# Kernel tuning notes

Measured on AMD Instinct MI355X. Metric: run time of the kernel, lower is better.

The kernel has to match this reference:

```python
import jax, jax.numpy as jnp
import numpy as np

N_NODES = 1_000_000
N_EDGES = 4_000_000
N_GRAPHS = 32768
IN_DIM, HID = 7, 128
BN_EPS = 1e-5


def setup_inputs() -> dict:
    key = jax.random.key(0)
    ks = iter(jax.random.split(key, 32))
    x = jax.random.normal(next(ks), (N_NODES, IN_DIM), jnp.float32)
    edge_index = jax.random.randint(next(ks), (2, N_EDGES), 0, N_NODES, dtype=jnp.int32)
    batch = jnp.sort(jax.random.randint(next(ks), (N_NODES,), 0, N_GRAPHS, dtype=jnp.int32))

    def lin_w(kk, fi, fo):  # torch nn.Linear-style init
        return (jax.random.uniform(kk, (fi, fo), jnp.float32) * 2.0 - 1.0) / np.float32(np.sqrt(fi))

    inp = {"x": x, "edge_index": edge_index, "batch": batch}
    dims = [(IN_DIM, HID), (HID, HID), (HID, HID)]
    for i, (fi, fo) in enumerate(dims, 1):
        inp[f"W{i}"] = lin_w(next(ks), fi, fo)
        inp[f"b{i}"] = jnp.zeros((fo,), jnp.float32)
        inp[f"gamma{i}"] = 1.0 + 0.1 * jax.random.normal(next(ks), (fo,), jnp.float32)
        inp[f"beta{i}"] = 0.1 * jax.random.normal(next(ks), (fo,), jnp.float32)
        inp[f"rmean{i}"] = jnp.zeros((fo,), jnp.float32)
        inp[f"rvar{i}"] = jnp.ones((fo,), jnp.float32)
    inp["Wc1"] = lin_w(next(ks), HID, HID // 2)
    inp["bc1"] = jnp.zeros((HID // 2,), jnp.float32)
    inp["Wc2"] = lin_w(next(ks), HID // 2, 1)
    inp["bc2"] = jnp.zeros((1,), jnp.float32)
    return inp


def _gcn_norm(edge_index, n):
    # PyG GCNConv: add self-loops, symmetric D^{-1/2} A D^{-1/2} normalization.
    loops = jnp.arange(n, dtype=edge_index.dtype)
    src = jnp.concatenate([edge_index[0], loops])
    dst = jnp.concatenate([edge_index[1], loops])
    deg = jax.ops.segment_sum(jnp.ones_like(dst, jnp.float32), dst, num_segments=n)
    dinv = jnp.where(deg > 0, jax.lax.rsqrt(deg), 0.0)
    return src, dst, dinv[src] * dinv[dst]


def reference(x, edge_index, batch,
              W1, b1, gamma1, beta1, rmean1, rvar1,
              W2, b2, gamma2, beta2, rmean2, rvar2,
              W3, b3, gamma3, beta3, rmean3, rvar3,
              Wc1, bc1, Wc2, bc2):
    n = x.shape[0]
    src, dst, norm = _gcn_norm(edge_index, n)
    layers = [(W1, b1, gamma1, beta1, rmean1, rvar1),
              (W2, b2, gamma2, beta2, rmean2, rvar2),
              (W3, b3, gamma3, beta3, rmean3, rvar3)]
    h = x
    for W, b, g, bt, rm, rv in layers:
        h = h @ W                                                   # [N, H]
        h = jax.ops.segment_sum(h[src] * norm[:, None], dst, num_segments=n) + b
        h = (h - rm) * jax.lax.rsqrt(rv + BN_EPS) * g + bt          # BatchNorm1d (eval)
        h = jax.nn.relu(h)                                          # dropout = identity in eval
    cnt = jax.ops.segment_sum(jnp.ones((n,), jnp.float32), batch, num_segments=N_GRAPHS)
    pooled = jax.ops.segment_sum(h, batch, num_segments=N_GRAPHS) / jnp.maximum(cnt, 1.0)[:, None]
    hidden = jax.nn.relu(pooled @ Wc1 + bc1)
    logits = (hidden @ Wc2 + bc2).squeeze(-1)                       # [N_GRAPHS]
    return logits
```

## Files before the change

kernel.cpp:

```cpp
#include <hip/hip_runtime.h>
#include <hip/hip_fp16.h>

#define N_NODES 1000000
#define N_EDGES 4000000
#define N_GRAPHS 32768
#define BN_EPS 1e-5f
#define NBLK1 3907

typedef _Float16 f16;
typedef f16   f16x8 __attribute__((ext_vector_type(8)));
typedef float f32x4 __attribute__((ext_vector_type(4)));
typedef float f32x2 __attribute__((ext_vector_type(2)));

__device__ __half g_hA[128000000];
__device__ __half g_hB[128000000];
__device__ float  g_agg7[8400000];
__device__ float  g_dinv[N_NODES];
__device__ int    g_rowcnt[N_NODES];
__device__ int    g_row_start[N_NODES + 1];
__device__ int    g_csr_src[N_EDGES];
__device__ int    g_part[NBLK1];
__device__ int    g_gstart[N_GRAPHS + 1];
__device__ __align__(16) __half g_wt1[4096];
__device__ __align__(16) __half g_wt2[16384];
__device__ __align__(16) __half g_wt3[16384];


__device__ __forceinline__ void set8(uint4 raw, float f[8]) {
    __half2 h; float2 a;
    __builtin_memcpy(&h, &raw.x, 4); a = __half22float2(h); f[0] = a.x; f[1] = a.y;
    __builtin_memcpy(&h, &raw.y, 4); a = __half22float2(h); f[2] = a.x; f[3] = a.y;
    __builtin_memcpy(&h, &raw.z, 4); a = __half22float2(h); f[4] = a.x; f[5] = a.y;
    __builtin_memcpy(&h, &raw.w, 4); a = __half22float2(h); f[6] = a.x; f[7] = a.y;
}
__device__ __forceinline__ uint4 pack8(const float f[8]) {
    __half2 h0 = __floats2half2_rn(f[0], f[1]);
    __half2 h1 = __floats2half2_rn(f[2], f[3]);
    __half2 h2 = __floats2half2_rn(f[4], f[5]);
    __half2 h3 = __floats2half2_rn(f[6], f[7]);
    uint4 raw;
    __builtin_memcpy(&raw.x, &h0, 4);
    __builtin_memcpy(&raw.y, &h1, 4);
    __builtin_memcpy(&raw.z, &h2, 4);
    __builtin_memcpy(&raw.w, &h3, 4);
    return raw;
}
__device__ __forceinline__ f32x2 cvt2h(unsigned raw) {
    __half2 h; __builtin_memcpy(&h, &raw, 4);
    float2 a = __half22float2(h);
    f32x2 r; r.x = a.x; r.y = a.y; return r;
}


__device__ __forceinline__ void set8_fp8v(uint2 raw, f32x2 f[4]) {
    f[0] = __builtin_amdgcn_cvt_pk_f32_fp8(raw.x, false);
    f[1] = __builtin_amdgcn_cvt_pk_f32_fp8(raw.x, true);
    f[2] = __builtin_amdgcn_cvt_pk_f32_fp8(raw.y, false);
    f[3] = __builtin_amdgcn_cvt_pk_f32_fp8(raw.y, true);
}
__device__ __forceinline__ void add8_fp8v(uint2 raw, f32x2 f[4]) {
    f[0] += __builtin_amdgcn_cvt_pk_f32_fp8(raw.x, false);
    f[1] += __builtin_amdgcn_cvt_pk_f32_fp8(raw.x, true);
    f[2] += __builtin_amdgcn_cvt_pk_f32_fp8(raw.y, false);
    f[3] += __builtin_amdgcn_cvt_pk_f32_fp8(raw.y, true);
}
__device__ __forceinline__ uint4 pack8v(const f32x2 f[4]) {
    __half2 h0 = __floats2half2_rn(f[0].x, f[0].y);
    __half2 h1 = __floats2half2_rn(f[1].x, f[1].y);
    __half2 h2 = __floats2half2_rn(f[2].x, f[2].y);
    __half2 h3 = __floats2half2_rn(f[3].x, f[3].y);
    uint4 raw;
    __builtin_memcpy(&raw.x, &h0, 4);
    __builtin_memcpy(&raw.y, &h1, 4);
    __builtin_memcpy(&raw.z, &h2, 4);
    __builtin_memcpy(&raw.w, &h3, 4);
    return raw;
}
__device__ __forceinline__ uint2 pack8_fp8(const float f[8]) {
    int lo = 0, hi = 0;
    lo = __builtin_amdgcn_cvt_pk_fp8_f32(f[0], f[1], lo, false);
    lo = __builtin_amdgcn_cvt_pk_fp8_f32(f[2], f[3], lo, true);
    hi = __builtin_amdgcn_cvt_pk_fp8_f32(f[4], f[5], hi, false);
    hi = __builtin_amdgcn_cvt_pk_fp8_f32(f[6], f[7], hi, true);
    uint2 r; r.x = (unsigned)lo; r.y = (unsigned)hi; return r;
}


__global__ __launch_bounds__(256) void k_prep(const float* __restrict__ W1,
                                              const float* __restrict__ W2,
                                              const float* __restrict__ W3) {
    int t = blockIdx.x * 256 + threadIdx.x;
    if (t < N_NODES) { g_rowcnt[t] = 0; return; }
    int u = t - N_NODES;
    if (u < 32768) {
        int sel = u >> 14, v = u & 16383;
        int n = v & 127, k = v >> 7;
        (sel ? g_wt3 : g_wt2)[n * 128 + k] = __float2half_rn((sel ? W3 : W2)[k * 128 + n]);
        return;
    }
    u -= 32768;
    if (u < 4096) {
        int n = u & 127, k = u >> 7;
        g_wt1[n * 32 + k] = (k < 7) ? __float2half_rn(W1[k * 128 + n]) : __float2half_rn(0.f);
    }
}


__global__ __launch_bounds__(256) void k_hist(const int* __restrict__ dst) {
    int e = blockIdx.x * 256 + threadIdx.x;
    if (e < N_EDGES) atomicAdd(&g_rowcnt[dst[e]], 1);
}

__global__ __launch_bounds__(256) void k_scan1(const float* __restrict__ x) {
    __shared__ int sh[256];
    int i = blockIdx.x * 256 + threadIdx.x;
    int v = (i < N_NODES) ? g_rowcnt[i] : 0;
    if (i < N_NODES) {
        float w = rsqrtf((float)(1 + v));
        g_dinv[i] = w;
        float vv[8];
#pragma unroll
        for (int k = 0; k < 7; ++k) vv[k] = x[i * 7 + k] * w;
        vv[7] = 0.f;
        *(uint4*)(g_hB + (size_t)i * 8) = pack8(vv);
    }
    sh[threadIdx.x] = v;
    __syncthreads();
#pragma unroll
    for (int off = 1; off < 256; off <<= 1) {
        int t = (threadIdx.x >= off) ? sh[threadIdx.x - off] : 0;
        __syncthreads();
        sh[threadIdx.x] += t;
        __syncthreads();
    }
    int incl = sh[threadIdx.x];
    if (i < N_NODES) g_row_start[i] = incl - v;
    if (threadIdx.x == 255) g_part[blockIdx.x] = incl;
}

__global__ __launch_bounds__(256) void k_scan2() {
    __shared__ int sh[256];
    int base = threadIdx.x * 16;
    int local[16];
    int s = 0;
#pragma unroll
    for (int k = 0; k < 16; ++k) {
        local[k] = (base + k < NBLK1) ? g_part[base + k] : 0;
        s += local[k];
    }
    sh[threadIdx.x] = s;
    __syncthreads();
#pragma unroll
    for (int off = 1; off < 256; off <<= 1) {
        int t = (threadIdx.x >= off) ? sh[threadIdx.x - off] : 0;
        __syncthreads();
        sh[threadIdx.x] += t;
        __syncthreads();
    }
    int carry = sh[threadIdx.x] - s;
#pragma unroll
    for (int k = 0; k < 16; ++k) {
        if (base + k < NBLK1) {
            int t = local[k];
            g_part[base + k] = carry;
            carry += t;
        }
    }
}

__global__ __launch_bounds__(256) void k_scan3() {
    int i = blockIdx.x * 256 + threadIdx.x;
    if (i < N_NODES) {
        g_row_start[i] += g_part[blockIdx.x];
        g_rowcnt[i] = 0;
    }
    if (i == 0) g_row_start[N_NODES] = N_EDGES;
}

__global__ __launch_bounds__(256) void k_scatter(const int* __restrict__ src,
                                                 const int* __restrict__ dst) {
    int e = blockIdx.x * 256 + threadIdx.x;
    if (e >= N_EDGES) return;
    int d = dst[e];
    int pos = g_row_start[d] + atomicAdd(&g_rowcnt[d], 1);
    g_csr_src[pos] = src[e];
}


__global__ __launch_bounds__(256) void k_gz(const int* __restrict__ batch) {
    int blk = blockIdx.x;
    if (blk < 4096) {
        int t = blk * 256 + threadIdx.x;
        *(float4*)(g_agg7 + (size_t)t * 4) = make_float4(0.f, 0.f, 0.f, 0.f);
        return;
    }
    int gidx = (blk - 4096) * 256 + threadIdx.x;
    if (gidx > N_GRAPHS) return;
    int lo = 0, hi = N_NODES;
    while (lo < hi) {
        int mid = (lo + hi) >> 1;
        if (batch[mid] < gidx) lo = mid + 1; else hi = mid;
    }
    g_gstart[gidx] = lo;
}


__global__ __launch_bounds__(256, 7) void k_l1_fused(const float* __restrict__ b,
                                                     const float* __restrict__ g,
                                                     const float* __restrict__ bt,
                                                     const float* __restrict__ rm,
                                                     const float* __restrict__ rv) {
    const __half* __restrict__ px = g_hB;
    unsigned char* __restrict__ q1 = (unsigned char*)g_hA;

    __shared__ __half As[64][152];
    const int tid = threadIdx.x;
    const int node0 = blockIdx.x * 64;

    {
        const int slot = tid >> 2;
        const int q = tid & 3;
        int i = node0 + slot;
        f32x2 f = cvt2h(*(const unsigned*)(px + (size_t)i * 8 + q * 2));
        int e = g_row_start[i], e1 = g_row_start[i + 1];
        for (; e + 4 <= e1; e += 4) {
            int s0 = g_csr_src[e + 0], s1 = g_csr_src[e + 1];
            int s2 = g_csr_src[e + 2], s3 = g_csr_src[e + 3];
            unsigned r0 = *(const unsigned*)(px + (size_t)s0 * 8 + q * 2);
            unsigned r1 = *(const unsigned*)(px + (size_t)s1 * 8 + q * 2);
            unsigned r2 = *(const unsigned*)(px + (size_t)s2 * 8 + q * 2);
            unsigned r3 = *(const unsigned*)(px + (size_t)s3 * 8 + q * 2);
            f += cvt2h(r0); f += cvt2h(r1); f += cvt2h(r2); f += cvt2h(r3);
        }
        for (; e < e1; ++e)
            f += cvt2h(*(const unsigned*)(px + (size_t)g_csr_src[e] * 8 + q * 2));
        __half2 hv = __floats2half2_rn(f.x, f.y);
        unsigned u; __builtin_memcpy(&u, &hv, 4);
        *(unsigned*)(&As[slot][q * 2]) = u;
        uint4 z; z.x = 0; z.y = 0; z.z = 0; z.w = 0;
        *(uint4*)(&As[slot][8 + q * 8]) = z;
    }

    const int wv = tid >> 6;
    const int lane = tid & 63;
    const int lm = lane & 15;
    const int lq = lane >> 4;

    __syncthreads();

    f32x4 acc[4][2];
#pragma unroll
    for (int mt = 0; mt < 4; ++mt)
#pragma unroll
        for (int nt = 0; nt < 2; ++nt) acc[mt][nt] = (f32x4){0.f, 0.f, 0.f, 0.f};

    f16x8 bq[2];
#pragma unroll
    for (int nt = 0; nt < 2; ++nt)
        __builtin_memcpy(&bq[nt], g_wt1 + (size_t)(wv * 32 + nt * 16 + lm) * 32 + lq * 8, 16);
#pragma unroll
    for (int mt = 0; mt < 4; ++mt) {
        f16x8 afr;
        __builtin_memcpy(&afr, &As[mt * 16 + lm][lq * 8], 16);
#pragma unroll
        for (int nt = 0; nt < 2; ++nt)
            acc[mt][nt] = __builtin_amdgcn_mfma_f32_16x16x32_f16(afr, bq[nt], acc[mt][nt], 0, 0, 0);
    }

    float4 dv4[4];
#pragma unroll
    for (int mt = 0; mt < 4; ++mt)
        dv4[mt] = *(const float4*)(g_dinv + node0 + mt * 16 + lq * 4);

    __syncthreads();

#pragma unroll
    for (int nt = 0; nt < 2; ++nt) {
        int c = wv * 32 + nt * 16 + lm;
        float s = g[c] * rsqrtf(rv[c] + BN_EPS);
        float o = fmaf(b[c] - rm[c], s, bt[c]);
#pragma unroll
        for (int mt = 0; mt < 4; ++mt) {
            float dvr[4] = {dv4[mt].x, dv4[mt].y, dv4[mt].z, dv4[mt].w};
#pragma unroll
            for (int r = 0; r < 4; ++r) {
                float y = fmaxf(fmaf(acc[mt][nt][r] * dvr[r], s, o), 0.f) * dvr[r];
                As[mt * 16 + lq * 4 + r][c] = __float2half_rn(y);
            }
        }
    }
    __syncthreads();
#pragma unroll
    for (int i = 0; i < 2; ++i) {
        int u = tid + i * 256;
        int row = u >> 3, cb = (u & 7) * 16;
        float fa[8], fb[8];
        set8(*(const uint4*)(&As[row][cb]), fa);
        set8(*(const uint4*)(&As[row][cb + 8]), fb);
        uint2 pa = pack8_fp8(fa), pb = pack8_fp8(fb);
        uint4 v; v.x = pa.x; v.y = pa.y; v.z = pb.x; v.w = pb.y;
        *(uint4*)(q1 + (size_t)(node0 + row) * 128 + cb) = v;
    }
}


template <bool PRE, bool ATOB, int WSEL, int OUTMODE>
__global__ __launch_bounds__(256, 7) void k_agg_gemm(const float* __restrict__ b,
                                                     const float* __restrict__ g,
                                                     const float* __restrict__ bt,
                                                     const float* __restrict__ rm,
                                                     const float* __restrict__ rv,
                                                     const int* __restrict__ batch) {
    const unsigned char* __restrict__ hin8 =
        (const unsigned char*)(ATOB ? g_hA : g_hB);
    unsigned char* __restrict__ hout8 =
        (unsigned char*)(ATOB ? g_hB : g_hA);
    const __half* __restrict__ WtG = (WSEL == 0) ? g_wt2 : g_wt3;

    __shared__ __half As[64][152];
    __shared__ int bsh[64];
    const int tid = threadIdx.x;
    const int node0 = blockIdx.x * 64;

    {
        const int slot = tid >> 4;
        const int c0 = (tid & 15) * 8;
#pragma unroll
        for (int pair = 0; pair < 2; ++pair) {
            const int iA = node0 + (pair * 2 + 0) * 16 + slot;
            const int iB = node0 + (pair * 2 + 1) * 16 + slot;
            f32x2 fA[4], fB[4];
            set8_fp8v(*(const uint2*)(hin8 + (size_t)iA * 128 + c0), fA);
            set8_fp8v(*(const uint2*)(hin8 + (size_t)iB * 128 + c0), fB);
            const int eA = g_row_start[iA], e1A = g_row_start[iA + 1];
            const int eB = g_row_start[iB], e1B = g_row_start[iB + 1];
            const int emA = min(max(e1A - 1, eA), N_EDGES - 1);
            const int emB = min(max(e1B - 1, eB), N_EDGES - 1);
            const int dmax = max(e1A - eA, e1B - eB);
            for (int done = 0; done < dmax; done += 4) {
                const int bA = eA + done, bB = eB + done;
                int sA0 = g_csr_src[min(bA,     emA)];
                int sA1 = g_csr_src[min(bA + 1, emA)];
                int sA2 = g_csr_src[min(bA + 2, emA)];
                int sA3 = g_csr_src[min(bA + 3, emA)];
                int sB0 = g_csr_src[min(bB,     emB)];
                int sB1 = g_csr_src[min(bB + 1, emB)];
                int sB2 = g_csr_src[min(bB + 2, emB)];
                int sB3 = g_csr_src[min(bB + 3, emB)];
                uint2 rA0 = *(const uint2*)(hin8 + (size_t)sA0 * 128 + c0);
                uint2 rA1 = *(const uint2*)(hin8 + (size_t)sA1 * 128 + c0);
                uint2 rA2 = *(const uint2*)(hin8 + (size_t)sA2 * 128 + c0);
                uint2 rA3 = *(const uint2*)(hin8 + (size_t)sA3 * 128 + c0);
                uint2 rB0 = *(const uint2*)(hin8 + (size_t)sB0 * 128 + c0);
                uint2 rB1 = *(const uint2*)(hin8 + (size_t)sB1 * 128 + c0);
                uint2 rB2 = *(const uint2*)(hin8 + (size_t)sB2 * 128 + c0);
                uint2 rB3 = *(const uint2*)(hin8 + (size_t)sB3 * 128 + c0);
                __builtin_amdgcn_sched_barrier(0);
                if (bA     >= e1A) { rA0.x = 0u; rA0.y = 0u; }
                if (bA + 1 >= e1A) { rA1.x = 0u; rA1.y = 0u; }
                if (bA + 2 >= e1A) { rA2.x = 0u; rA2.y = 0u; }
                if (bA + 3 >= e1A) { rA3.x = 0u; rA3.y = 0u; }
                if (bB     >= e1B) { rB0.x = 0u; rB0.y = 0u; }
                if (bB + 1 >= e1B) { rB1.x = 0u; rB1.y = 0u; }
                if (bB + 2 >= e1B) { rB2.x = 0u; rB2.y = 0u; }
                if (bB + 3 >= e1B) { rB3.x = 0u; rB3.y = 0u; }
                add8_fp8v(rA0, fA); add8_fp8v(rA1, fA); add8_fp8v(rA2, fA); add8_fp8v(rA3, fA);
                add8_fp8v(rB0, fB); add8_fp8v(rB1, fB); add8_fp8v(rB2, fB); add8_fp8v(rB3, fB);
            }
            *(uint4*)(&As[(pair * 2 + 0) * 16 + slot][c0]) = pack8v(fA);
            *(uint4*)(&As[(pair * 2 + 1) * 16 + slot][c0]) = pack8v(fB);
        }
    }

    const int wv = tid >> 6;
    const int lane = tid & 63;
    const int lm = lane & 15;
    const int lq = lane >> 4;

    __syncthreads();

    f32x4 acc[4][2];
#pragma unroll
    for (int mt = 0; mt < 4; ++mt)
#pragma unroll
        for (int nt = 0; nt < 2; ++nt) acc[mt][nt] = (f32x4){0.f, 0.f, 0.f, 0.f};

#pragma unroll
    for (int kb = 0; kb < 4; ++kb) {
        f16x8 bq[2];
#pragma unroll
        for (int nt = 0; nt < 2; ++nt)
            __builtin_memcpy(&bq[nt],
                             WtG + (size_t)(wv * 32 + nt * 16 + lm) * 128 + kb * 32 + lq * 8, 16);
#pragma unroll
        for (int mt = 0; mt < 4; ++mt) {
            f16x8 afr;
            __builtin_memcpy(&afr, &As[mt * 16 + lm][kb * 32 + lq * 8], 16);
#pragma unroll
            for (int nt = 0; nt < 2; ++nt)
                acc[mt][nt] = __builtin_amdgcn_mfma_f32_16x16x32_f16(afr, bq[nt], acc[mt][nt], 0, 0, 0);
        }
    }

    float4 dv4[4];
#pragma unroll
    for (int mt = 0; mt < 4; ++mt)
        dv4[mt] = *(const float4*)(g_dinv + node0 + mt * 16 + lq * 4);

    if (OUTMODE == 2 && tid < 64) bsh[tid] = batch[node0 + tid];

    __syncthreads();

#pragma unroll
    for (int nt = 0; nt < 2; ++nt) {
        int c = wv * 32 + nt * 16 + lm;
        float s = g[c] * rsqrtf(rv[c] + BN_EPS);
        float o = fmaf(b[c] - rm[c], s, bt[c]);
#pragma unroll
        for (int mt = 0; mt < 4; ++mt) {
            float dvr[4] = {dv4[mt].x, dv4[mt].y, dv4[mt].z, dv4[mt].w};
#pragma unroll
            for (int r = 0; r < 4; ++r) {
                float pm = PRE ? dvr[r] : 1.0f;
                float y = fmaxf(fmaf(acc[mt][nt][r] * dvr[r], s, o), 0.f) * pm;
                As[mt * 16 + lq * 4 + r][c] = __float2half_rn(y);
            }
        }
    }
    __syncthreads();

    if (OUTMODE == 1) {
#pragma unroll
        for (int i = 0; i < 2; ++i) {
            int u = tid + i * 256;
            int row = u >> 3, cb = (u & 7) * 16;
            float fa[8], fb[8];
            set8(*(const uint4*)(&As[row][cb]), fa);
            set8(*(const uint4*)(&As[row][cb + 8]), fb);
            uint2 pa = pack8_fp8(fa), pb = pack8_fp8(fb);
            uint4 v; v.x = pa.x; v.y = pa.y; v.z = pb.x; v.w = pb.y;
            *(uint4*)(hout8 + (size_t)(node0 + row) * 128 + cb) = v;
        }
    } else {
        const int c = tid & 127;
        const int r0 = (tid >> 7) * 32;
        float accp = 0.f;
        int g0 = bsh[r0];
        for (int row = r0; row < r0 + 32; ++row) {
            int gg = bsh[row];
            if (gg != g0) {
                atomicAdd(&g_agg7[(size_t)g0 * 128 + c], accp);
                accp = 0.f; g0 = gg;
            }
            accp += __half2float(As[row][c]);
        }
        atomicAdd(&g_agg7[(size_t)g0 * 128 + c], accp);
    }
}


__global__ __launch_bounds__(256) void k_head(const float* __restrict__ Wc1,
                                              const float* __restrict__ bc1,
                                              const float* __restrict__ Wc2,
                                              const float* __restrict__ bc2,
                                              float* __restrict__ out) {
    __shared__ float hsh[4][64];
    const int g4 = blockIdx.x * 4;
    const int gi = g4 + (threadIdx.x >> 6);
    const int c = threadIdx.x & 63;
    const float* pooled = g_agg7;
    int cnt = g_gstart[gi + 1] - g_gstart[gi];
    float inv = 1.0f / (float)max(cnt, 1);
    float z = 0.f;
#pragma unroll 8
    for (int k = 0; k < 128; ++k) z = fmaf(pooled[(size_t)gi * 128 + k], Wc1[k * 64 + c], z);
    hsh[threadIdx.x >> 6][c] = fmaxf(fmaf(z, inv, bc1[c]), 0.f);
    __syncthreads();
    if (threadIdx.x < 4) {
        float zz = bc2[0];
#pragma unroll 8
        for (int k = 0; k < 64; ++k) zz = fmaf(hsh[threadIdx.x][k], Wc2[k], zz);
        out[g4 + threadIdx.x] = zz;
    }
}


extern "C" void kernel_launch(void* const* d_in, const int* in_sizes, int n_in,
                              void* d_out, int out_size, void* d_ws, size_t ws_size,
                              hipStream_t stream) {
    const float* x     = (const float*)d_in[0];
    const int*   ei    = (const int*)d_in[1];
    const int*   batch = (const int*)d_in[2];
    const float* W1 = (const float*)d_in[3];
    const float* b1 = (const float*)d_in[4];
    const float* g1 = (const float*)d_in[5];
    const float* bt1= (const float*)d_in[6];
    const float* rm1= (const float*)d_in[7];
    const float* rv1= (const float*)d_in[8];
    const float* W2 = (const float*)d_in[9];
    const float* b2 = (const float*)d_in[10];
    const float* g2 = (const float*)d_in[11];
    const float* bt2= (const float*)d_in[12];
    const float* rm2= (const float*)d_in[13];
    const float* rv2= (const float*)d_in[14];
    const float* W3 = (const float*)d_in[15];
    const float* b3 = (const float*)d_in[16];
    const float* g3 = (const float*)d_in[17];
    const float* bt3= (const float*)d_in[18];
    const float* rm3= (const float*)d_in[19];
    const float* rv3= (const float*)d_in[20];
    const float* Wc1= (const float*)d_in[21];
    const float* bc1= (const float*)d_in[22];
    const float* Wc2= (const float*)d_in[23];
    const float* bc2= (const float*)d_in[24];
    float* outp = (float*)d_out;
    (void)d_ws; (void)ws_size; (void)n_in; (void)in_sizes;

    const int* srcp = ei;
    const int* dstp = ei + N_EDGES;

    k_prep<<<4051, 256, 0, stream>>>(W1, W2, W3);

    k_hist<<<(N_EDGES + 255) / 256, 256, 0, stream>>>(dstp);
    k_scan1<<<NBLK1, 256, 0, stream>>>(x);
    k_scan2<<<1, 256, 0, stream>>>();
    k_scan3<<<NBLK1, 256, 0, stream>>>();
    k_scatter<<<(N_EDGES + 255) / 256, 256, 0, stream>>>(srcp, dstp);

    k_gz<<<4225, 256, 0, stream>>>(batch);

    k_l1_fused<<<N_NODES / 64, 256, 0, stream>>>(b1, g1, bt1, rm1, rv1);

    k_agg_gemm<true,  true,  0, 1><<<N_NODES / 64, 256, 0, stream>>>(b2, g2, bt2, rm2, rv2, batch);
    k_agg_gemm<false, false, 1, 2><<<N_NODES / 64, 256, 0, stream>>>(b3, g3, bt3, rm3, rv3, batch);

    k_head<<<N_GRAPHS / 4, 256, 0, stream>>>(Wc1, bc1, Wc2, bc2, outp);
}
```

Measured before the change: 1.062 ms.

## Build CSR via two-level bucket sort with shared-memory atomics

Replaces the global-atomic histogram and scatter used for CSR construction with a two-pass bucketed approach. Edges are first binned into 256 coarse destination buckets, using block-local lists and then global appends. Per-bucket blocks then count degrees and place sources using shared-memory atomics. The aim is to cut scattered global atomics and random writes, at the cost of an extra packed-pair buffer and more kernel launches. Only 256 blocks run the per-bucket kernels, which limits parallelism on a large GPU.

```diff
diff --git a/kernel.cpp b/kernel.cpp
--- a/kernel.cpp
+++ b/kernel.cpp
@@ -6,6 +6,11 @@
 #define N_GRAPHS 32768
 #define BN_EPS 1e-5f
 #define NBLK1 3907
+#define NB 256
+#define BKT_SHIFT 12
+#define EPB 2048
+#define NSCAT 1954
+#define CAPB 32
 
 typedef _Float16 f16;
 typedef f16   f16x8 __attribute__((ext_vector_type(8)));
@@ -19,8 +24,12 @@
 __device__ int    g_rowcnt[N_NODES];
 __device__ int    g_row_start[N_NODES + 1];
 __device__ int    g_csr_src[N_EDGES];
+__device__ unsigned g_pairs[N_EDGES];
 __device__ int    g_part[NBLK1];
 __device__ int    g_gstart[N_GRAPHS + 1];
+__device__ int    g_bcnt[NB];
+__device__ int    g_bstart[NB + 1];
+__device__ int    g_bcur[NB];
 __device__ __align__(16) __half g_wt1[4096];
 __device__ __align__(16) __half g_wt2[16384];
 __device__ __align__(16) __half g_wt3[16384];
@@ -102,13 +111,104 @@
     if (u < 4096) {
         int n = u & 127, k = u >> 7;
         g_wt1[n * 32 + k] = (k < 7) ? __float2half_rn(W1[k * 128 + n]) : __float2half_rn(0.f);
-    }
-}
-
-
-__global__ __launch_bounds__(256) void k_hist(const int* __restrict__ dst) {
-    int e = blockIdx.x * 256 + threadIdx.x;
-    if (e < N_EDGES) atomicAdd(&g_rowcnt[dst[e]], 1);
+        return;
+    }
+    u -= 4096;
+    if (u < NB) g_bcnt[u] = 0;
+}
+
+
+__global__ __launch_bounds__(256) void k_bhist(const int* __restrict__ dst) {
+    __shared__ int h[NB];
+    h[threadIdx.x] = 0;
+    __syncthreads();
+    int base = blockIdx.x * EPB;
+#pragma unroll
+    for (int k = 0; k < 8; ++k) {
+        int e = base + k * 256 + threadIdx.x;
+        if (e < N_EDGES) atomicAdd(&h[((unsigned)dst[e]) >> BKT_SHIFT], 1);
+    }
+    __syncthreads();
+    int c = h[threadIdx.x];
+    if (c) atomicAdd(&g_bcnt[threadIdx.x], c);
+}
+
+__global__ __launch_bounds__(256) void k_bscan() {
+    __shared__ int sh[256];
+    int v = g_bcnt[threadIdx.x];
+    sh[threadIdx.x] = v;
+    __syncthreads();
+#pragma unroll
+    for (int off = 1; off < 256; off <<= 1) {
+        int t = (threadIdx.x >= off) ? sh[threadIdx.x - off] : 0;
+        __syncthreads();
+        sh[threadIdx.x] += t;
+        __syncthreads();
+    }
+    int excl = sh[threadIdx.x] - v;
+    g_bstart[threadIdx.x] = excl;
+    g_bcur[threadIdx.x] = excl;
+    if (threadIdx.x == 255) g_bstart[NB] = N_EDGES;
+}
+
+__global__ __launch_bounds__(256) void k_bscatter(const int* __restrict__ src,
+                                                  const int* __restrict__ dst) {
+    __shared__ int lcnt[NB];
+    __shared__ unsigned llist[NB][CAPB];
+    lcnt[threadIdx.x] = 0;
+    __syncthreads();
+    int base = blockIdx.x * EPB;
+#pragma unroll
+    for (int k = 0; k < 8; ++k) {
+        int e = base + k * 256 + threadIdx.x;
+        if (e < N_EDGES) {
+            unsigned d = (unsigned)dst[e];
+            unsigned p = (((unsigned)src[e]) << BKT_SHIFT) | (d & 4095u);
+            int b = (int)(d >> BKT_SHIFT);
+            int slot = atomicAdd(&lcnt[b], 1);
+            if (slot < CAPB) llist[b][slot] = p;
+            else {
+                int gpos = atomicAdd(&g_bcur[b], 1);
+                g_pairs[gpos] = p;
+            }
+        }
+    }
+    __syncthreads();
+    int c = min(lcnt[threadIdx.x], CAPB);
+    if (c > 0) {
+        int gbase = atomicAdd(&g_bcur[threadIdx.x], c);
+        for (int i = 0; i < c; ++i) g_pairs[gbase + i] = llist[threadIdx.x][i];
+    }
+}
+
+__global__ __launch_bounds__(256) void k_bdeg() {
+    __shared__ int cnt[4096];
+    const int b = blockIdx.x;
+    for (int j = threadIdx.x; j < 4096; j += 256) cnt[j] = 0;
+    __syncthreads();
+    const int s0 = g_bstart[b], s1 = g_bstart[b + 1];
+    for (int i = s0 + threadIdx.x; i < s1; i += 256)
+        atomicAdd(&cnt[g_pairs[i] & 4095u], 1);
+    __syncthreads();
+    const int n0 = b << BKT_SHIFT;
+    for (int j = threadIdx.x; j < 4096; j += 256)
+        if (n0 + j < N_NODES) g_rowcnt[n0 + j] = cnt[j];
+}
+
+__global__ __launch_bounds__(256) void k_bcsr() {
+    __shared__ int cnt[4096];
+    const int b = blockIdx.x;
+    for (int j = threadIdx.x; j < 4096; j += 256) cnt[j] = 0;
+    __syncthreads();
+    const int s0 = g_bstart[b], s1 = g_bstart[b + 1];
+    const int n0 = b << BKT_SHIFT;
+    for (int i = s0 + threadIdx.x; i < s1; i += 256) {
+        unsigned p = g_pairs[i];
+        int dl = (int)(p & 4095u);
+        int off = atomicAdd(&cnt[dl], 1);
+        int pos = g_row_start[n0 + dl] + off;
+        g_csr_src[pos] = (int)(p >> BKT_SHIFT);
+    }
 }
 
 __global__ __launch_bounds__(256) void k_scan1(const float* __restrict__ x) {
@@ -170,20 +270,8 @@
 
 __global__ __launch_bounds__(256) void k_scan3() {
     int i = blockIdx.x * 256 + threadIdx.x;
-    if (i < N_NODES) {
-        g_row_start[i] += g_part[blockIdx.x];
-        g_rowcnt[i] = 0;
-    }
+    if (i < N_NODES) g_row_start[i] += g_part[blockIdx.x];
     if (i == 0) g_row_start[N_NODES] = N_EDGES;
-}
-
-__global__ __launch_bounds__(256) void k_scatter(const int* __restrict__ src,
-                                                 const int* __restrict__ dst) {
-    int e = blockIdx.x * 256 + threadIdx.x;
-    if (e >= N_EDGES) return;
-    int d = dst[e];
-    int pos = g_row_start[d] + atomicAdd(&g_rowcnt[d], 1);
-    g_csr_src[pos] = src[e];
 }
 
 
@@ -519,13 +607,18 @@
     const int* srcp = ei;
     const int* dstp = ei + N_EDGES;
 
-    k_prep<<<4051, 256, 0, stream>>>(W1, W2, W3);
-
-    k_hist<<<(N_EDGES + 255) / 256, 256, 0, stream>>>(dstp);
+    k_prep<<<4052, 256, 0, stream>>>(W1, W2, W3);
+
+    k_bhist<<<NSCAT, 256, 0, stream>>>(dstp);
+    k_bscan<<<1, 256, 0, stream>>>();
+    k_bscatter<<<NSCAT, 256, 0, stream>>>(srcp, dstp);
+    k_bdeg<<<NB, 256, 0, stream>>>();
+
     k_scan1<<<NBLK1, 256, 0, stream>>>(x);
     k_scan2<<<1, 256, 0, stream>>>();
     k_scan3<<<NBLK1, 256, 0, stream>>>();
-    k_scatter<<<(N_EDGES + 255) / 256, 256, 0, stream>>>(srcp, dstp);
+
+    k_bcsr<<<NB, 256, 0, stream>>>();
 
     k_gz<<<4225, 256, 0, stream>>>(batch);
 
```

Result: faster. 910.1 us (-14.3%).
